# Performance work log

Hardware: AMD Instinct MI355X
Metric: run time of the kernel (lower is better)

Reference implementation:

```python
import jax, jax.numpy as jnp
import numpy as np


def _conv3x3_relu(x, w, b):
    # 3x3 conv, padding 1 (SAME), NCHW / OIHW, then ReLU (Conv2d with activation=ReLU)
    y = jax.lax.conv_general_dilated(x, w, (1, 1), ((1, 1), (1, 1)),
                                     dimension_numbers=('NCHW', 'OIHW', 'NCHW'))
    return jax.nn.relu(y + b[None, :, None, None])


def _forward(features, cnn_w, cnn_b, gcn_w, gcn_b, up_w, up_b,
             deconv_w, deconv_b, pred_w, pred_b):
    # ---- CNN stack (mask_fcn1..4) ----
    x = features
    for i in range(cnn_w.shape[0]):
        x = _conv3x3_relu(x, cnn_w[i], cnn_b[i])

    B, C, H, W = x.shape
    N = H * W  # pixels = graph nodes per ROI

    # ---- cosine-similarity adjacency per sample ----
    f = x.reshape(B, C, N).transpose(0, 2, 1)          # [B, N, C] node features
    norms = jnp.linalg.norm(f, axis=-1, keepdims=True)
    fn = f / jnp.maximum(norms, 1e-8)
    A = jnp.einsum('bnc,bmc->bnm', fn, fn)             # [B, N, N]

    # ---- symmetric GCN normalization with self-loops: D^-1/2 (A+I) D^-1/2 ----
    A = A + jnp.eye(N, dtype=A.dtype)[None]
    d = jnp.sum(A, axis=-1)                            # [B, N]
    dinv = jax.lax.rsqrt(jnp.maximum(d, 1e-12))
    A = A * dinv[:, :, None] * dinv[:, None, :]

    # ---- GCN layers: x' = A_hat @ (x W) + b, then GELU ----
    g = f
    for i in range(gcn_w.shape[0]):
        g = jnp.einsum('bnm,bmc->bnc', A, g @ gcn_w[i]) + gcn_b[i]
        g = jax.nn.gelu(g, approximate=False)

    x = g.transpose(0, 2, 1).reshape(B, C, H, W)

    # ---- Upsample head ----
    for i in range(up_w.shape[0]):
        x = _conv3x3_relu(x, up_w[i], up_b[i])
    feats = x  # returned roi_features, [B, C, H, W]

    # ConvTranspose2d(k=2, s=2): dilated conv with flipped, IO-swapped kernel
    wt = jnp.flip(deconv_w, (2, 3)).transpose(1, 0, 2, 3)  # (out, in, 2, 2)
    y = jax.lax.conv_general_dilated(feats, wt, (1, 1), ((1, 1), (1, 1)),
                                     lhs_dilation=(2, 2),
                                     dimension_numbers=('NCHW', 'OIHW', 'NCHW'))
    y = jax.nn.relu(y + deconv_b[None, :, None, None])    # [B, C, 2H, 2W]

    mask = jax.lax.conv_general_dilated(y, pred_w, (1, 1), ((0, 0), (0, 0)),
                                        dimension_numbers=('NCHW', 'OIHW', 'NCHW'))
    mask = mask + pred_b[None, :, None, None]             # [B, num_classes, 2H, 2W]
    return mask, feats


def setup_inputs() -> dict:
    key = jax.random.key(0)
    ks = jax.random.split(key, 12)
    B, C, H, W, NC = 512, 256, 14, 14, 80

    def p(k, shape, s=0.05):
        return jax.random.normal(k, shape, jnp.float32) * s

    return {
        'features': jax.random.normal(ks[0], (B, C, H, W), jnp.float32),
        'cnn_w': p(ks[1], (4, C, C, 3, 3)),
        'cnn_b': p(ks[2], (4, C)),
        'gcn_w': p(ks[3], (2, C, C)),
        'gcn_b': p(ks[4], (2, C)),
        'up_w': p(ks[5], (2, C, C, 3, 3)),
        'up_b': p(ks[6], (2, C)),
        'deconv_w': p(ks[7], (C, C, 2, 2)),  # PyTorch ConvTranspose2d layout (in, out, kH, kW)
        'deconv_b': p(ks[8], (C,)),
        'pred_w': p(ks[9], (NC, C, 1, 1)),
        'pred_b': p(ks[10], (NC,)),
    }


def reference(features, cnn_w, cnn_b, gcn_w, gcn_b, up_w, up_b,
              deconv_w, deconv_b, pred_w, pred_b):
    return _forward(features, cnn_w, cnn_b, gcn_w, gcn_b, up_w, up_b,
                    deconv_w, deconv_b, pred_w, pred_b)
```

## Files before the change

kernel.cpp:

```cpp
#include <hip/hip_runtime.h>
#include <stdint.h>

typedef __attribute__((ext_vector_type(8))) short short8;
typedef __attribute__((ext_vector_type(4))) float f32x4;

#define B_N   512
#define NPIX  196
#define MTOT  (B_N*NPIX)
#define NPAD  224

static_assert(MTOT % 128 == 0, "M must tile by 128");

__device__ __forceinline__ float bf2f(unsigned short u){
  unsigned int x = ((unsigned int)u) << 16;
  return __builtin_bit_cast(float, x);
}
__device__ __forceinline__ unsigned short f2bf(float f){
  unsigned int x = __builtin_bit_cast(unsigned int, f);
  x += 0x7fffu + ((x >> 16) & 1u);
  return (unsigned short)(x >> 16);
}
__device__ __forceinline__ void gload16(const void* g, void* l){
  __builtin_amdgcn_global_load_lds(
    (const __attribute__((address_space(1))) void*)(uintptr_t)g,
    (__attribute__((address_space(3))) void*)(uintptr_t)l, 16, 0, 0);
}
__device__ __forceinline__ float gelu_exact(float x){
  return 0.5f * x * (1.f + erff(x * 0.70710678118654752440f));
}

template<int EPI>
__global__ __launch_bounds__(256, 3) void gemm_conv(
    const unsigned short* __restrict__ A, const unsigned short* __restrict__ Bt,
    unsigned short* __restrict__ outb, float* __restrict__ outf,
    const float* __restrict__ bias)
{
  __shared__ __align__(16) char smem[2*10240];
  const int tid = threadIdx.x;
  const int wid = tid >> 6, lane = tid & 63;
  const int wr = wid >> 1, wc = wid & 1;
  const int orig = blockIdx.x;
  const int vid = (orig & 7) * 196 + (orig >> 3);
  const int m0 = (vid >> 1) * 128;
  const int nb = vid & 1;

  const int ssw = ((lane & 3) ^ ((lane >> 3) & 3)) << 4;
  const int s16 = (lane >> 4) << 4;

  auto stageA = [&](int cc, char* dst){
#pragma unroll
    for (int s = 0; s < 3; ++s) {
      const int g = wid + s*4;
      if (g < 10) {
        const int r = g*16 + (lane >> 2);
        long gr = (long)m0 - 16 + r;
        if (gr < 0) gr = 0;
        if (gr >= MTOT) gr = MTOT - 1;
        gload16((const char*)A + (size_t)gr*512 + (size_t)cc*64 + (size_t)ssw,
                dst + g*1024);
      }
    }
  };

  f32x4 acc[4][4];
#pragma unroll
  for (int i=0;i<4;i++)
#pragma unroll
    for (int j=0;j<4;j++) acc[i][j] = (f32x4){0.f,0.f,0.f,0.f};

  int arow[4]; unsigned hh[4], ww[4];
#pragma unroll
  for (int i=0;i<4;i++){
    const int ml = wr*64 + i*16 + (lane&15);
    arow[i] = ml + 16;
    const int p = (m0 + ml) % NPIX;
    hh[i] = (unsigned)(p / 14); ww[i] = (unsigned)(p % 14);
  }
  const short8 zero8 = {0,0,0,0,0,0,0,0};

  const unsigned short* bbase = Bt + ((size_t)(nb*8 + wc*4)*64 + lane)*8;

  stageA(0, smem);
  __syncthreads();

#pragma unroll 1
  for (int c = 0; c < 8; ++c) {
    if (c < 7) stageA(c+1, smem + ((c+1)&1)*10240);
    const char* aB = smem + (c&1)*10240;
#pragma unroll 3
    for (int tap = 0; tap < 9; ++tap) {
      const unsigned short* bp = bbase + (size_t)(tap*8 + c)*8192;
      short8 bv[4];
#pragma unroll
      for (int j=0;j<4;j++) bv[j] = *(const short8*)(bp + j*512);
      const int dh = tap/3 - 1, dw = tap - (tap/3)*3 - 1;
      const int doff = dh*14 + dw;
      short8 av[4];
#pragma unroll
      for (int i=0;i<4;i++){
        const int r = arow[i] + doff;
        short8 a = *(const short8*)(aB + r*64 + (s16 ^ (((r>>1)&3)<<4)));
        const bool val = (hh[i] + (unsigned)dh < 14u) && (ww[i] + (unsigned)dw < 14u);
        av[i] = val ? a : zero8;
      }
#pragma unroll
      for (int i=0;i<4;i++)
#pragma unroll
        for (int j=0;j<4;j++)
          acc[i][j] = __builtin_amdgcn_mfma_f32_16x16x32_bf16(av[i], bv[j], acc[i][j], 0,0,0);
    }
    __syncthreads();
  }

#pragma unroll
  for (int i=0;i<4;i++){
#pragma unroll
    for (int j=0;j<4;j++){
#pragma unroll
      for (int r=0;r<4;r++){
        const int row = m0 + wr*64 + i*16 + ((lane>>4)<<2) + r;
        const int col = nb*128 + wc*64 + j*16 + (lane&15);
        float v = acc[i][j][r] + bias[col];
        v = fmaxf(v, 0.f);
        outb[(size_t)row*256 + col] = f2bf(v);
        if constexpr (EPI == 1) {
          const int b = row / NPIX, p = row - b*NPIX;
          outf[((size_t)b*256 + col)*NPIX + p] = v;
        }
      }
    }
  }
}

template<int KI, int EPI>
__global__ __launch_bounds__(256) void gemm_g(
    const unsigned short* __restrict__ A, const unsigned short* __restrict__ Bt,
    unsigned short* __restrict__ outb, float* __restrict__ outf,
    const float* __restrict__ bias, int th, int tw)
{
  __shared__ __align__(16) char smem[16384];
  char* sA = smem; char* sB = smem + 8192;
  const int tid = threadIdx.x;
  const int wid = tid >> 6, lane = tid & 63;
  const int wr = wid >> 1, wc = wid & 1;
  const int m0 = blockIdx.x * 128, n0 = blockIdx.y * 128;
  const int rs = wid*16 + (lane >> 2);
  const int ssw = ((lane & 3) ^ ((lane >> 3) & 3)) << 4;
  char* dA0 = sA + wid*1024; char* dA1 = sA + 4096 + wid*1024;
  char* dB0 = sB + wid*1024; char* dB1 = sB + 4096 + wid*1024;
  const char* pA0 = (const char*)(A + (size_t)(m0 + rs)      * (KI*32));
  const char* pA1 = (const char*)(A + (size_t)(m0 + rs + 64) * (KI*32));
  const char* pB0 = (const char*)(Bt + (size_t)(n0 + rs)      * (KI*32));
  const char* pB1 = (const char*)(Bt + (size_t)(n0 + rs + 64) * (KI*32));

  f32x4 acc[4][4];
#pragma unroll
  for (int i=0;i<4;i++)
#pragma unroll
    for (int j=0;j<4;j++) acc[i][j] = (f32x4){0.f,0.f,0.f,0.f};

  const int s16 = (lane >> 4) << 4;

#pragma unroll 1
  for (int kk = 0; kk < KI; ++kk) {
    const int ko = kk*64 + ssw;
    gload16(pA0 + ko, dA0);
    gload16(pA1 + ko, dA1);
    gload16(pB0 + ko, dB0);
    gload16(pB1 + ko, dB1);
    __syncthreads();
    short8 av[4], bv[4];
#pragma unroll
    for (int i=0;i<4;i++){
      const int ra = wr*64 + i*16 + (lane&15);
      const int rb = wc*64 + i*16 + (lane&15);
      av[i] = *(const short8*)(sA + ra*64 + (s16 ^ (((ra>>1)&3)<<4)));
      bv[i] = *(const short8*)(sB + rb*64 + (s16 ^ (((rb>>1)&3)<<4)));
    }
#pragma unroll
    for (int i=0;i<4;i++)
#pragma unroll
      for (int j=0;j<4;j++)
        acc[i][j] = __builtin_amdgcn_mfma_f32_16x16x32_bf16(av[i], bv[j], acc[i][j], 0,0,0);
    __syncthreads();
  }

#pragma unroll
  for (int i=0;i<4;i++){
#pragma unroll
    for (int j=0;j<4;j++){
#pragma unroll
      for (int r=0;r<4;r++){
        const int row = m0 + wr*64 + i*16 + ((lane>>4)<<2) + r;
        const int col = n0 + wc*64 + j*16 + (lane&15);
        float v = acc[i][j][r];
        if constexpr (EPI == 0) {
          v += bias[col];
          v = fmaxf(v, 0.f);
          outb[(size_t)row*256 + col] = f2bf(v);
        } else if constexpr (EPI == 2) {
          const int b = row / NPIX, p = row - b*NPIX;
          outb[((size_t)b*256 + col)*NPAD + p] = f2bf(v);
        } else if constexpr (EPI == 3) {
          if (col < 80) {
            const int b = row / NPIX, p = row - b*NPIX;
            const int h = p / 14, w = p - h*14;
            outf[(((size_t)b*80 + col)*28 + (2*h + th))*28 + (2*w + tw)] = v + bias[col];
          }
        }
      }
    }
  }
}

template<int EPI, int KI>
__global__ __launch_bounds__(256) void gemm_s(
    const unsigned short* __restrict__ Asrc, int a_rps, int a_stride, long amax,
    const unsigned short* __restrict__ Bsrc, int b_rps, int b_stride, long bmax,
    unsigned short* __restrict__ outb, const float* __restrict__ bias)
{
  __shared__ __align__(16) char smem[16384];
  char* sA = smem; char* sB = smem + 8192;
  const int tid = threadIdx.x;
  const int wid = tid >> 6, lane = tid & 63;
  const int wr = wid >> 1, wc = wid & 1;
  const int m0 = blockIdx.x * 128, n0 = blockIdx.y * 128;
  const int b  = blockIdx.z;
  const int rs = wid*16 + (lane >> 2);
  const int ssw = ((lane & 3) ^ ((lane >> 3) & 3)) << 4;
  char* dA0 = sA + wid*1024; char* dA1 = sA + 4096 + wid*1024;
  char* dB0 = sB + wid*1024; char* dB1 = sB + 4096 + wid*1024;
  long ar0 = (long)b*a_rps + m0 + rs;       if (ar0 > amax) ar0 = amax;
  long ar1 = (long)b*a_rps + m0 + rs + 64;  if (ar1 > amax) ar1 = amax;
  long br0 = (long)b*b_rps + n0 + rs;       if (br0 > bmax) br0 = bmax;
  long br1 = (long)b*b_rps + n0 + rs + 64;  if (br1 > bmax) br1 = bmax;
  const char* pA0  = (const char*)(Asrc + ar0 * a_stride);
  const char* pA1  = (const char*)(Asrc + ar1 * a_stride);
  const char* pBt0 = (const char*)(Bsrc + br0 * b_stride);
  const char* pBt1 = (const char*)(Bsrc + br1 * b_stride);

  f32x4 acc[4][4];
#pragma unroll
  for (int i=0;i<4;i++)
#pragma unroll
    for (int j=0;j<4;j++) acc[i][j] = (f32x4){0.f,0.f,0.f,0.f};

  const int s16 = (lane >> 4) << 4;

#pragma unroll 1
  for (int kk = 0; kk < KI; ++kk) {
    const int ko = kk*64 + ssw;
    gload16(pA0 + ko, dA0);
    gload16(pA1 + ko, dA1);
    gload16(pBt0 + ko, dB0);
    gload16(pBt1 + ko, dB1);
    __syncthreads();
    short8 av[4], bv[4];
#pragma unroll
    for (int i=0;i<4;i++){
      const int ra = wr*64 + i*16 + (lane&15);
      const int rb = wc*64 + i*16 + (lane&15);
      av[i] = *(const short8*)(sA + ra*64 + (s16 ^ (((ra>>1)&3)<<4)));
      bv[i] = *(const short8*)(sB + rb*64 + (s16 ^ (((rb>>1)&3)<<4)));
    }
#pragma unroll
    for (int i=0;i<4;i++)
#pragma unroll
      for (int j=0;j<4;j++)
        acc[i][j] = __builtin_amdgcn_mfma_f32_16x16x32_bf16(av[i], bv[j], acc[i][j], 0,0,0);
    __syncthreads();
  }

#pragma unroll
  for (int i=0;i<4;i++){
#pragma unroll
    for (int j=0;j<4;j++){
#pragma unroll
      for (int r=0;r<4;r++){
        const int ml = m0 + wr*64 + i*16 + ((lane>>4)<<2) + r;
        const int nl = n0 + wc*64 + j*16 + (lane&15);
        const float v = acc[i][j][r];
        if constexpr (EPI == 4) {
          if (ml < NPAD && nl < NPAD) {
            const float o = (ml < NPIX && nl < NPIX) ? v : 0.f;
            outb[((size_t)b*NPAD + ml)*NPAD + nl] = f2bf(o);
          }
        } else {
          if (ml < NPIX) {
            const float x = v + bias[nl];
            outb[((size_t)b*NPIX + ml)*256 + nl] = f2bf(gelu_exact(x));
          }
        }
      }
    }
  }
}


__global__ void k_tin(const float* __restrict__ in, unsigned short* __restrict__ out)
{
  __shared__ float t[32][29];
  const int b = blockIdx.x, p0 = blockIdx.y * 28, c0 = blockIdx.z * 32;
  const int tid = threadIdx.x;
  for (int i = tid; i < 896; i += 256) {
    const int c = i / 28, p = i - c*28;
    t[c][p] = in[((size_t)b*256 + c0 + c)*196 + p0 + p];
  }
  __syncthreads();
  for (int i = tid; i < 896; i += 256) {
    const int p = i >> 5, c = i & 31;
    out[((size_t)b*196 + p0 + p)*256 + c0 + c] = f2bf(t[c][p]);
  }
}

__global__ void k_fnnorm(const unsigned short* __restrict__ f, unsigned short* __restrict__ fn)
{
  const int row  = blockIdx.x * 4 + (threadIdx.x >> 6);
  const int lane = threadIdx.x & 63;
  const unsigned short* src = f + (size_t)row*256 + lane*4;
  const float x0 = bf2f(src[0]), x1 = bf2f(src[1]), x2 = bf2f(src[2]), x3 = bf2f(src[3]);
  float s = x0*x0 + x1*x1 + x2*x2 + x3*x3;
#pragma unroll
  for (int o = 32; o > 0; o >>= 1) s += __shfl_xor(s, o, 64);
  const float scale = 1.f / fmaxf(sqrtf(s), 1e-8f);
  unsigned short* dst = fn + (size_t)row*256 + lane*4;
  dst[0]=f2bf(x0*scale); dst[1]=f2bf(x1*scale); dst[2]=f2bf(x2*scale); dst[3]=f2bf(x3*scale);
}

__global__ void k_rowsum(const unsigned short* __restrict__ Ahat, float* __restrict__ dinv)
{
  const int b = blockIdx.x, n = threadIdx.x;
  if (n >= NPAD) return;
  const unsigned short* base = Ahat + (size_t)b*NPAD*NPAD + n;
  float s = 0.f;
  for (int m = 0; m < NPAD; ++m) s += bf2f(base[(size_t)m*NPAD]);
  dinv[b*NPAD + n] = rsqrtf(fmaxf(s + 1.f, 1e-12f));
}

__global__ void k_anorm(unsigned short* __restrict__ Ahat, const float* __restrict__ dinv)
{
  const size_t idx = (size_t)blockIdx.x * 256 + threadIdx.x;
  const int m = (int)(idx % NPAD);
  const size_t t2 = idx / NPAD;
  const int n = (int)(t2 % NPAD);
  const int b = (int)(t2 / NPAD);
  float v = bf2f(Ahat[idx]);
  if (n == m && n < NPIX) v += 1.f;
  v *= dinv[b*NPAD + n] * dinv[b*NPAD + m];
  Ahat[idx] = f2bf(v);
}

__global__ void k_prep(const float* __restrict__ cnn_w, const float* __restrict__ up_w,
                       const float* __restrict__ gcn_w, const float* __restrict__ dec_w,
                       const float* __restrict__ pred_w,
                       unsigned short* __restrict__ bt_cnn, unsigned short* __restrict__ bt_up,
                       unsigned short* __restrict__ bt_gcn, unsigned short* __restrict__ bt_dec,
                       unsigned short* __restrict__ bt_pred, unsigned short* __restrict__ zbuf,
                       unsigned short* __restrict__ tcm)
{
  long i = (long)blockIdx.x * 256 + threadIdx.x;
  long n = 4L*589824;
  if (i < n) {
    const long l = i / 589824, r = i % 589824;
    const long tap = r >> 16, r2 = r & 65535;
    const long c = r2 >> 13, n16 = (r2 >> 9) & 15, kchunk = (r2 >> 7) & 3;
    const long nl = (r2 >> 3) & 15, ke = r2 & 7;
    const long co = n16*16 + nl, ci = c*32 + kchunk*8 + ke;
    bt_cnn[i] = f2bf(cnn_w[(((l*256+co)*256+ci)*3 + tap/3)*3 + (tap%3)]);
    return;
  }
  i -= n; n = 2L*589824;
  if (i < n) {
    const long l = i / 589824, r = i % 589824;
    const long tap = r >> 16, r2 = r & 65535;
    const long c = r2 >> 13, n16 = (r2 >> 9) & 15, kchunk = (r2 >> 7) & 3;
    const long nl = (r2 >> 3) & 15, ke = r2 & 7;
    const long co = n16*16 + nl, ci = c*32 + kchunk*8 + ke;
    bt_up[i] = f2bf(up_w[(((l*256+co)*256+ci)*3 + tap/3)*3 + (tap%3)]);
    return;
  }
  i -= n; n = 2L*256*256;
  if (i < n) {
    const long ci = i & 255, co = (i >> 8) & 255, l = i >> 16;
    bt_gcn[i] = f2bf(gcn_w[(l*256 + ci)*256 + co]);
    return;
  }
  i -= n; n = 4L*256*256;
  if (i < n) {
    const long ci = i & 255, co = (i >> 8) & 255, t = i >> 16;
    bt_dec[i] = f2bf(dec_w[((ci*256 + co)*2 + (t>>1))*2 + (t&1)]);
    return;
  }
  i -= n; n = 128L*256;
  if (i < n) {
    const long co = i & 255, k = i >> 8;
    bt_pred[i] = (k < 80) ? f2bf(pred_w[k*256 + co]) : (unsigned short)0;
    return;
  }
  i -= n; n = 2048;
  if (i < n) { zbuf[i] = 0; return; }
  i -= n; n = 512L*256*28;
  if (i < n) {
    const long p = 196 + (i % 28);
    const long rest = i / 28;
    const long c = rest & 255, bb = rest >> 8;
    tcm[((size_t)(bb*256 + c))*NPAD + p] = 0;
    return;
  }
}

extern "C" void kernel_launch(void* const* d_in, const int* in_sizes, int n_in,
                              void* d_out, int out_size, void* d_ws, size_t ws_size,
                              hipStream_t stream)
{
  const float* features = (const float*)d_in[0];
  const float* cnn_w  = (const float*)d_in[1];
  const float* cnn_b  = (const float*)d_in[2];
  const float* gcn_w  = (const float*)d_in[3];
  const float* gcn_b  = (const float*)d_in[4];
  const float* up_w   = (const float*)d_in[5];
  const float* up_b   = (const float*)d_in[6];
  const float* dec_w  = (const float*)d_in[7];
  const float* dec_b  = (const float*)d_in[8];
  const float* pred_w = (const float*)d_in[9];
  const float* pred_b = (const float*)d_in[10];

  char* ws = (char*)d_ws;
  size_t o = 0;
  auto take = [&](size_t nbytes) -> char* {
    char* p = ws + o;
    o += (nbytes + 255) & ~(size_t)255;
    return p;
  };
  unsigned short* bt_cnn  = (unsigned short*)take(4L*589824*2);
  unsigned short* bt_up   = (unsigned short*)take(2L*589824*2);
  unsigned short* bt_gcn  = (unsigned short*)take(2L*256*256*2);
  unsigned short* bt_dec  = (unsigned short*)take(4L*256*256*2);
  unsigned short* bt_pred = (unsigned short*)take(128L*256*2);
  unsigned short* zbuf    = (unsigned short*)take(4096);
  unsigned short* actA    = (unsigned short*)take((size_t)MTOT*256*2);
  unsigned short* actB    = (unsigned short*)take((size_t)MTOT*256*2);
  unsigned short* ahat    = (unsigned short*)take((size_t)B_N*NPAD*NPAD*2);
  unsigned short* tcm     = (unsigned short*)take((size_t)B_N*256*NPAD*2);
  float*          dinv    = (float*)take((size_t)B_N*NPAD*4);
  (void)zbuf;

  float* mask  = (float*)d_out;
  float* feats = mask + (size_t)B_N*80*28*28;

  const dim3 blk(256);
  const dim3 gc(1568);
  const dim3 gg(MTOT/128, 2);
  const dim3 gs(2, 2, B_N);

  k_prep<<<29832, blk, 0, stream>>>(cnn_w, up_w, gcn_w, dec_w, pred_w,
                                    bt_cnn, bt_up, bt_gcn, bt_dec, bt_pred, zbuf, tcm);
  k_tin<<<dim3(B_N, 7, 8), blk, 0, stream>>>(features, actA);

  gemm_conv<0><<<gc, blk, 0, stream>>>(actA, bt_cnn + 0L*589824, actB, nullptr, cnn_b + 0);
  gemm_conv<0><<<gc, blk, 0, stream>>>(actB, bt_cnn + 1L*589824, actA, nullptr, cnn_b + 256);
  gemm_conv<0><<<gc, blk, 0, stream>>>(actA, bt_cnn + 2L*589824, actB, nullptr, cnn_b + 512);
  gemm_conv<0><<<gc, blk, 0, stream>>>(actB, bt_cnn + 3L*589824, actA, nullptr, cnn_b + 768);

  k_fnnorm<<<MTOT/4, blk, 0, stream>>>(actA, actB);
  gemm_s<4,8><<<gs, blk, 0, stream>>>(actB, NPIX, 256, (long)MTOT-1,
                                      actB, NPIX, 256, (long)MTOT-1, ahat, nullptr);
  k_rowsum<<<B_N, blk, 0, stream>>>(ahat, dinv);
  k_anorm<<<100352, blk, 0, stream>>>(ahat, dinv);

  gemm_g<8,2><<<gg, blk, 0, stream>>>(actA, bt_gcn, tcm, nullptr, nullptr, 0,0);
  gemm_s<5,7><<<gs, blk, 0, stream>>>(ahat, NPAD, NPAD, (long)B_N*NPAD-1,
                                      tcm, 256, NPAD, (long)B_N*256-1, actB, gcn_b);
  gemm_g<8,2><<<gg, blk, 0, stream>>>(actB, bt_gcn + 65536, tcm, nullptr, nullptr, 0,0);
  gemm_s<5,7><<<gs, blk, 0, stream>>>(ahat, NPAD, NPAD, (long)B_N*NPAD-1,
                                      tcm, 256, NPAD, (long)B_N*256-1, actA, gcn_b + 256);

  gemm_conv<0><<<gc, blk, 0, stream>>>(actA, bt_up + 0L*589824, actB, nullptr, up_b + 0);
  gemm_conv<1><<<gc, blk, 0, stream>>>(actB, bt_up + 1L*589824, actA, feats,   up_b + 256);

  unsigned short* ybuf = ahat;
  for (int t = 0; t < 4; ++t) {
    gemm_g<8,0><<<gg, blk, 0, stream>>>(actA, bt_dec + (long)t*65536, ybuf, nullptr, dec_b, 0,0);
    gemm_g<8,3><<<dim3(MTOT/128, 1), blk, 0, stream>>>(ybuf, bt_pred, nullptr, mask, pred_b, t>>1, t&1);
  }
}
```

Baseline: 1.586 ms.

## Fuse deconv+pred into one kernel and compute GCN degrees algebraically

Replaces the four deconv/pred GEMM launch pairs with one fused kernel that keeps the deconv output tile in LDS and feeds it straight into the 1x1 prediction GEMM, avoiding the intermediate global round trip. It also computes the adjacency degrees as fn·(sum of fn) before the similarity GEMM and folds the self-loop and D^-1/2 scaling into that GEMM's epilogue, which removes the rowsum and normalize passes over the NxN matrix. The conv kernel now reads a zeroed LDS slot for out-of-bounds taps instead of selecting a zero vector. The degrees now come from fp32 sums of bf16 features rather than of the bf16-rounded adjacency, so numerics change slightly.

```diff
diff --git a/kernel.cpp b/kernel.cpp
--- a/kernel.cpp
+++ b/kernel.cpp
@@ -35,7 +35,7 @@
     unsigned short* __restrict__ outb, float* __restrict__ outf,
     const float* __restrict__ bias)
 {
-  __shared__ __align__(16) char smem[2*10240];
+  __shared__ __align__(16) char smem[2*10240 + 64];
   const int tid = threadIdx.x;
   const int wid = tid >> 6, lane = tid & 63;
   const int wr = wid >> 1, wc = wid & 1;
@@ -46,6 +46,8 @@
 
   const int ssw = ((lane & 3) ^ ((lane >> 3) & 3)) << 4;
   const int s16 = (lane >> 4) << 4;
+
+  if (tid < 16) ((int*)(smem + 20480))[tid] = 0;
 
   auto stageA = [&](int cc, char* dst){
 #pragma unroll
@@ -76,9 +78,9 @@
     const int p = (m0 + ml) % NPIX;
     hh[i] = (unsigned)(p / 14); ww[i] = (unsigned)(p % 14);
   }
-  const short8 zero8 = {0,0,0,0,0,0,0,0};
 
   const unsigned short* bbase = Bt + ((size_t)(nb*8 + wc*4)*64 + lane)*8;
+  const char* pz = smem + 20480 + s16;
 
   stageA(0, smem);
   __syncthreads();
@@ -99,9 +101,9 @@
 #pragma unroll
       for (int i=0;i<4;i++){
         const int r = arow[i] + doff;
-        short8 a = *(const short8*)(aB + r*64 + (s16 ^ (((r>>1)&3)<<4)));
+        const char* pa = aB + r*64 + (s16 ^ (((r>>1)&3)<<4));
         const bool val = (hh[i] + (unsigned)dh < 14u) && (ww[i] + (unsigned)dw < 14u);
-        av[i] = val ? a : zero8;
+        av[i] = *(const short8*)(val ? pa : pz);
       }
 #pragma unroll
       for (int i=0;i<4;i++)
@@ -129,6 +131,127 @@
         }
       }
     }
+  }
+}
+
+__global__ __launch_bounds__(512) void k_decpred(
+    const unsigned short* __restrict__ A, const unsigned short* __restrict__ Bdec,
+    const unsigned short* __restrict__ Bpred, const float* __restrict__ decb,
+    const float* __restrict__ predb, float* __restrict__ mask)
+{
+  __shared__ __align__(16) char smem[49152];
+  char* sA = smem;
+  char* sD = smem + 32768;
+  const int tid = threadIdx.x;
+  const int wid = tid >> 6, lane = tid & 63;
+  const int m0 = blockIdx.x * 64;
+  const int ssw = ((lane & 3) ^ ((lane >> 3) & 3)) << 4;
+  const int s16 = (lane >> 4) << 4;
+  const int wr = wid >> 2, wn = wid & 3;
+
+#pragma unroll
+  for (int p = 0; p < 4; ++p) {
+    const int cc = p*2 + (wid >> 2);
+    const int r  = (wid & 3)*16 + (lane >> 2);
+    gload16((const char*)A + (size_t)(m0 + r)*512 + (size_t)cc*64 + (size_t)ssw,
+            sA + cc*4096 + (wid & 3)*1024);
+  }
+
+  float bd[4];
+#pragma unroll
+  for (int j = 0; j < 4; ++j) bd[j] = decb[wn*64 + j*16 + (lane & 15)];
+  float pb[2]; int pcol[2];
+#pragma unroll
+  for (int j = 0; j < 2; ++j) {
+    pcol[j] = wn*32 + j*16 + (lane & 15);
+    pb[j] = (pcol[j] < 80) ? predb[pcol[j]] : 0.f;
+  }
+
+  __syncthreads();
+
+#pragma unroll 1
+  for (int tap = 0; tap < 4; ++tap) {
+    f32x4 acc[2][4];
+#pragma unroll
+    for (int i=0;i<2;i++)
+#pragma unroll
+      for (int j=0;j<4;j++) acc[i][j] = (f32x4){0.f,0.f,0.f,0.f};
+#pragma unroll
+    for (int c = 0; c < 8; ++c) {
+      short8 bv[4];
+#pragma unroll
+      for (int j=0;j<4;j++)
+        bv[j] = *(const short8*)(Bdec + (size_t)((tap*8+c)*16 + wn*4+j)*512 + lane*8);
+      short8 av[2];
+#pragma unroll
+      for (int i=0;i<2;i++){
+        const int rA = wr*32 + i*16 + (lane&15);
+        av[i] = *(const short8*)(sA + c*4096 + rA*64 + (s16 ^ (((rA>>1)&3)<<4)));
+      }
+#pragma unroll
+      for (int i=0;i<2;i++)
+#pragma unroll
+        for (int j=0;j<4;j++)
+          acc[i][j] = __builtin_amdgcn_mfma_f32_16x16x32_bf16(av[i], bv[j], acc[i][j],0,0,0);
+    }
+
+    f32x4 acc2[2][2];
+#pragma unroll
+    for (int i=0;i<2;i++)
+#pragma unroll
+      for (int j=0;j<2;j++) acc2[i][j] = (f32x4){0.f,0.f,0.f,0.f};
+
+#pragma unroll 1
+    for (int h = 0; h < 2; ++h) {
+      if ((wn >> 1) == h) {
+#pragma unroll
+        for (int i=0;i<2;i++)
+#pragma unroll
+          for (int j=0;j<4;j++)
+#pragma unroll
+            for (int rr=0;rr<4;rr++){
+              const int row = wr*32 + i*16 + ((lane>>4)<<2) + rr;
+              const int colL = (wn&1)*64 + j*16 + (lane&15);
+              const float v = fmaxf(acc[i][j][rr] + bd[j], 0.f);
+              *(unsigned short*)(sD + row*256 + (((colL>>3) ^ (row&7))<<4)
+                                 + ((colL<<1)&15)) = f2bf(v);
+            }
+      }
+      __syncthreads();
+#pragma unroll
+      for (int c = 0; c < 4; ++c) {
+        short8 bp2[2];
+#pragma unroll
+        for (int j=0;j<2;j++)
+          bp2[j] = *(const short8*)(Bpred + (size_t)((h*4+c)*8 + wn*2+j)*512 + lane*8);
+        short8 ap[2];
+#pragma unroll
+        for (int i=0;i<2;i++){
+          const int rP = wr*32 + i*16 + (lane&15);
+          ap[i] = *(const short8*)(sD + rP*256 + (((c*4 + (lane>>4)) ^ (rP&7))<<4));
+        }
+#pragma unroll
+        for (int i=0;i<2;i++)
+#pragma unroll
+          for (int j=0;j<2;j++)
+            acc2[i][j] = __builtin_amdgcn_mfma_f32_16x16x32_bf16(ap[i], bp2[j], acc2[i][j],0,0,0);
+      }
+      __syncthreads();
+    }
+#pragma unroll
+    for (int i=0;i<2;i++)
+#pragma unroll
+      for (int j=0;j<2;j++)
+#pragma unroll
+        for (int rr=0;rr<4;rr++){
+          if (pcol[j] < 80) {
+            const int row = m0 + wr*32 + i*16 + ((lane>>4)<<2) + rr;
+            const int b = row / NPIX, p = row - b*NPIX;
+            const int hh = p/14, ww2 = p - hh*14;
+            mask[(((size_t)b*80 + pcol[j])*28 + 2*hh + (tap>>1))*28 + 2*ww2 + (tap&1)]
+                = acc2[i][j][rr] + pb[j];
+          }
+        }
   }
 }
 
@@ -201,12 +324,6 @@
         } else if constexpr (EPI == 2) {
           const int b = row / NPIX, p = row - b*NPIX;
           outb[((size_t)b*256 + col)*NPAD + p] = f2bf(v);
-        } else if constexpr (EPI == 3) {
-          if (col < 80) {
-            const int b = row / NPIX, p = row - b*NPIX;
-            const int h = p / 14, w = p - h*14;
-            outf[(((size_t)b*80 + col)*28 + (2*h + th))*28 + (2*w + tw)] = v + bias[col];
-          }
         }
       }
     }
@@ -271,23 +388,41 @@
     __syncthreads();
   }
 
-#pragma unroll
-  for (int i=0;i<4;i++){
+  if constexpr (EPI == 4) {
+    int nlv[4]; float dn[4];
 #pragma unroll
     for (int j=0;j<4;j++){
+      nlv[j] = n0 + wc*64 + j*16 + (lane&15);
+      dn[j] = (nlv[j] < NPIX) ? bias[(size_t)b*NPIX + nlv[j]] : 0.f;
+    }
+#pragma unroll
+    for (int i=0;i<4;i++){
 #pragma unroll
       for (int r=0;r<4;r++){
         const int ml = m0 + wr*64 + i*16 + ((lane>>4)<<2) + r;
-        const int nl = n0 + wc*64 + j*16 + (lane&15);
-        const float v = acc[i][j][r];
-        if constexpr (EPI == 4) {
-          if (ml < NPAD && nl < NPAD) {
-            const float o = (ml < NPIX && nl < NPIX) ? v : 0.f;
-            outb[((size_t)b*NPAD + ml)*NPAD + nl] = f2bf(o);
+        const float dmv = (ml < NPIX) ? bias[(size_t)b*NPIX + ml] : 0.f;
+        if (ml < NPAD) {
+#pragma unroll
+          for (int j=0;j<4;j++){
+            if (nlv[j] < NPAD) {
+              const float o = (acc[i][j][r] + ((ml==nlv[j]) ? 1.f : 0.f)) * dmv * dn[j];
+              outb[((size_t)b*NPAD + ml)*NPAD + nlv[j]] = f2bf(o);
+            }
           }
-        } else {
+        }
+      }
+    }
+  } else {
+#pragma unroll
+    for (int i=0;i<4;i++){
+#pragma unroll
+      for (int j=0;j<4;j++){
+#pragma unroll
+        for (int r=0;r<4;r++){
+          const int ml = m0 + wr*64 + i*16 + ((lane>>4)<<2) + r;
+          const int nl = n0 + wc*64 + j*16 + (lane&15);
           if (ml < NPIX) {
-            const float x = v + bias[nl];
+            const float x = acc[i][j][r] + bias[nl];
             outb[((size_t)b*NPIX + ml)*256 + nl] = f2bf(gelu_exact(x));
           }
         }
@@ -327,27 +462,27 @@
   dst[0]=f2bf(x0*scale); dst[1]=f2bf(x1*scale); dst[2]=f2bf(x2*scale); dst[3]=f2bf(x3*scale);
 }
 
-__global__ void k_rowsum(const unsigned short* __restrict__ Ahat, float* __restrict__ dinv)
-{
-  const int b = blockIdx.x, n = threadIdx.x;
-  if (n >= NPAD) return;
-  const unsigned short* base = Ahat + (size_t)b*NPAD*NPAD + n;
+__global__ void k_ssum(const unsigned short* __restrict__ fn, float* __restrict__ S)
+{
+  const int b = blockIdx.x, c = threadIdx.x;
+  const unsigned short* p = fn + (size_t)b*NPIX*256 + c;
   float s = 0.f;
-  for (int m = 0; m < NPAD; ++m) s += bf2f(base[(size_t)m*NPAD]);
-  dinv[b*NPAD + n] = rsqrtf(fmaxf(s + 1.f, 1e-12f));
-}
-
-__global__ void k_anorm(unsigned short* __restrict__ Ahat, const float* __restrict__ dinv)
-{
-  const size_t idx = (size_t)blockIdx.x * 256 + threadIdx.x;
-  const int m = (int)(idx % NPAD);
-  const size_t t2 = idx / NPAD;
-  const int n = (int)(t2 % NPAD);
-  const int b = (int)(t2 / NPAD);
-  float v = bf2f(Ahat[idx]);
-  if (n == m && n < NPIX) v += 1.f;
-  v *= dinv[b*NPAD + n] * dinv[b*NPAD + m];
-  Ahat[idx] = f2bf(v);
+  for (int i = 0; i < NPIX; ++i) s += bf2f(p[(size_t)i*256]);
+  S[b*256 + c] = s;
+}
+
+__global__ void k_dinv(const unsigned short* __restrict__ fn, const float* __restrict__ S,
+                       float* __restrict__ dinv)
+{
+  const int row  = blockIdx.x * 4 + (threadIdx.x >> 6);
+  const int lane = threadIdx.x & 63;
+  const int b = row / NPIX;
+  const unsigned short* p = fn + (size_t)row*256 + lane*4;
+  const float* sp = S + b*256 + lane*4;
+  float d = bf2f(p[0])*sp[0] + bf2f(p[1])*sp[1] + bf2f(p[2])*sp[2] + bf2f(p[3])*sp[3];
+#pragma unroll
+  for (int o = 32; o > 0; o >>= 1) d += __shfl_xor(d, o, 64);
+  if (lane == 0) dinv[row] = rsqrtf(fmaxf(d + 1.f, 1e-12f));
 }
 
 __global__ void k_prep(const float* __restrict__ cnn_w, const float* __restrict__ up_w,
@@ -355,8 +490,7 @@
                        const float* __restrict__ pred_w,
                        unsigned short* __restrict__ bt_cnn, unsigned short* __restrict__ bt_up,
                        unsigned short* __restrict__ bt_gcn, unsigned short* __restrict__ bt_dec,
-                       unsigned short* __restrict__ bt_pred, unsigned short* __restrict__ zbuf,
-                       unsigned short* __restrict__ tcm)
+                       unsigned short* __restrict__ bt_pred, unsigned short* __restrict__ tcm)
 {
   long i = (long)blockIdx.x * 256 + threadIdx.x;
   long n = 4L*589824;
@@ -385,20 +519,21 @@
     bt_gcn[i] = f2bf(gcn_w[(l*256 + ci)*256 + co]);
     return;
   }
-  i -= n; n = 4L*256*256;
+  i -= n; n = 262144;
   if (i < n) {
-    const long ci = i & 255, co = (i >> 8) & 255, t = i >> 16;
-    bt_dec[i] = f2bf(dec_w[((ci*256 + co)*2 + (t>>1))*2 + (t&1)]);
+    const long ke = i&7, nl = (i>>3)&15, k4 = (i>>7)&3, g = (i>>9)&15;
+    const long c = (i>>13)&7, tap = i>>16;
+    const long co = g*16 + nl, ci = c*32 + k4*8 + ke;
+    bt_dec[i] = f2bf(dec_w[((ci*256 + co)*2 + (tap>>1))*2 + (tap&1)]);
     return;
   }
-  i -= n; n = 128L*256;
+  i -= n; n = 32768;
   if (i < n) {
-    const long co = i & 255, k = i >> 8;
-    bt_pred[i] = (k < 80) ? f2bf(pred_w[k*256 + co]) : (unsigned short)0;
+    const long ke = i&7, nl = (i>>3)&15, k4 = (i>>7)&3, g = (i>>9)&7, c = i>>12;
+    const long cls = g*16 + nl, ci = c*32 + k4*8 + ke;
+    bt_pred[i] = (cls < 80) ? f2bf(pred_w[cls*256 + ci]) : (unsigned short)0;
     return;
   }
-  i -= n; n = 2048;
-  if (i < n) { zbuf[i] = 0; return; }
   i -= n; n = 512L*256*28;
   if (i < n) {
     const long p = 196 + (i % 28);
@@ -435,15 +570,14 @@
   unsigned short* bt_cnn  = (unsigned short*)take(4L*589824*2);
   unsigned short* bt_up   = (unsigned short*)take(2L*589824*2);
   unsigned short* bt_gcn  = (unsigned short*)take(2L*256*256*2);
-  unsigned short* bt_dec  = (unsigned short*)take(4L*256*256*2);
-  unsigned short* bt_pred = (unsigned short*)take(128L*256*2);
-  unsigned short* zbuf    = (unsigned short*)take(4096);
+  unsigned short* bt_dec  = (unsigned short*)take(262144L*2);
+  unsigned short* bt_pred = (unsigned short*)take(32768L*2);
   unsigned short* actA    = (unsigned short*)take((size_t)MTOT*256*2);
   unsigned short* actB    = (unsigned short*)take((size_t)MTOT*256*2);
   unsigned short* ahat    = (unsigned short*)take((size_t)B_N*NPAD*NPAD*2);
   unsigned short* tcm     = (unsigned short*)take((size_t)B_N*256*NPAD*2);
-  float*          dinv    = (float*)take((size_t)B_N*NPAD*4);
-  (void)zbuf;
+  float*          Sbuf    = (float*)take((size_t)B_N*256*4);
+  float*          dinvb   = (float*)take((size_t)MTOT*4);
 
   float* mask  = (float*)d_out;
   float* feats = mask + (size_t)B_N*80*28*28;
@@ -453,8 +587,8 @@
   const dim3 gg(MTOT/128, 2);
   const dim3 gs(2, 2, B_N);
 
-  k_prep<<<29832, blk, 0, stream>>>(cnn_w, up_w, gcn_w, dec_w, pred_w,
-                                    bt_cnn, bt_up, bt_gcn, bt_dec, bt_pred, zbuf, tcm);
+  k_prep<<<29824, blk, 0, stream>>>(cnn_w, up_w, gcn_w, dec_w, pred_w,
+                                    bt_cnn, bt_up, bt_gcn, bt_dec, bt_pred, tcm);
   k_tin<<<dim3(B_N, 7, 8), blk, 0, stream>>>(features, actA);
 
   gemm_conv<0><<<gc, blk, 0, stream>>>(actA, bt_cnn + 0L*589824, actB, nullptr, cnn_b + 0);
@@ -463,10 +597,10 @@
   gemm_conv<0><<<gc, blk, 0, stream>>>(actB, bt_cnn + 3L*589824, actA, nullptr, cnn_b + 768);
 
   k_fnnorm<<<MTOT/4, blk, 0, stream>>>(actA, actB);
+  k_ssum<<<B_N, blk, 0, stream>>>(actB, Sbuf);
+  k_dinv<<<MTOT/4, blk, 0, stream>>>(actB, Sbuf, dinvb);
   gemm_s<4,8><<<gs, blk, 0, stream>>>(actB, NPIX, 256, (long)MTOT-1,
-                                      actB, NPIX, 256, (long)MTOT-1, ahat, nullptr);
-  k_rowsum<<<B_N, blk, 0, stream>>>(ahat, dinv);
-  k_anorm<<<100352, blk, 0, stream>>>(ahat, dinv);
+                                      actB, NPIX, 256, (long)MTOT-1, ahat, dinvb);
 
   gemm_g<8,2><<<gg, blk, 0, stream>>>(actA, bt_gcn, tcm, nullptr, nullptr, 0,0);
   gemm_s<5,7><<<gs, blk, 0, stream>>>(ahat, NPAD, NPAD, (long)B_N*NPAD-1,
@@ -478,9 +612,6 @@
   gemm_conv<0><<<gc, blk, 0, stream>>>(actA, bt_up + 0L*589824, actB, nullptr, up_b + 0);
   gemm_conv<1><<<gc, blk, 0, stream>>>(actB, bt_up + 1L*589824, actA, feats,   up_b + 256);
 
-  unsigned short* ybuf = ahat;
-  for (int t = 0; t < 4; ++t) {
-    gemm_g<8,0><<<gg, blk, 0, stream>>>(actA, bt_dec + (long)t*65536, ybuf, nullptr, dec_b, 0,0);
-    gemm_g<8,3><<<dim3(MTOT/128, 1), blk, 0, stream>>>(ybuf, bt_pred, nullptr, mask, pred_b, t>>1, t&1);
-  }
-}
+  k_decpred<<<dim3(MTOT/64), dim3(512), 0, stream>>>(actA, bt_dec, bt_pred,
+                                                     dec_b, pred_b, mask);
+}
```

Result: faster. 1.455 ms (-8.3%).
